# Kernel tuning notes

Measured on AMD Instinct MI355X. Metric: run time of the kernel, lower is better.

## Reference

```python
import jax, jax.numpy as jnp
import numpy as np

SIGMA = 1.0


def _sq_dists(a, b):
    # ||a_i - b_j||^2 via gemm: (n_a, n_b)
    aa = jnp.sum(a * a, axis=1)[:, None]
    bb = jnp.sum(b * b, axis=1)[None, :]
    ab = a @ b.T
    return jnp.maximum(aa + bb - 2.0 * ab, 0.0)


def _rbf(a, b, sigma):
    return jnp.exp(-_sq_dists(a, b) / (2.0 * sigma * sigma))


def setup_inputs() -> dict:
    key = jax.random.key(0)
    kx, ky = jax.random.split(key)
    x = jax.random.normal(kx, (4096, 1024), dtype=jnp.float32)
    y = jax.random.normal(ky, (4096, 1024), dtype=jnp.float32)
    return {"x": x, "y": y}


def reference(x, y):
    # Flatten non-batch dims (module accepts (n, f1, f2, ...))
    xf = x.reshape(x.shape[0], -1)
    yf = y.reshape(y.shape[0], -1)
    n = xf.shape[0]
    m = yf.shape[0]

    k_xx = _rbf(xf, xf, SIGMA)
    k_yy = _rbf(yf, yf, SIGMA)
    k_xy = _rbf(xf, yf, SIGMA)

    # Unbiased estimator: exclude diagonal of k_xx / k_yy
    sum_xx = jnp.sum(k_xx) - jnp.trace(k_xx)
    sum_yy = jnp.sum(k_yy) - jnp.trace(k_yy)
    sum_xy = jnp.sum(k_xy)

    mmd2 = (sum_xx / (n * (n - 1))
            + sum_yy / (m * (m - 1))
            - 2.0 * sum_xy / (n * m))
    return mmd2
```

## Files before the change

### kernel.cpp

```cpp
#include <hip/hip_runtime.h>


#define NROWS 4096
#define KDIM  1024
#define BM 128
#define BN 256
#define NTI 32
#define NTJ 16
#define XY  512
#define TRIB 272

typedef unsigned short u16;
typedef unsigned char  u8;
typedef __attribute__((ext_vector_type(8))) int   int8v;
typedef __attribute__((ext_vector_type(4))) int   int4v;
typedef __attribute__((ext_vector_type(8))) short short8;
typedef __attribute__((ext_vector_type(4))) float f32x4;

__global__ void mmd_zero_sums(float* sums) {
    if (threadIdx.x < 3) sums[threadIdx.x] = 0.0f;
}

__device__ __forceinline__ void async_copy16(const void* g, void* l) {
    __builtin_amdgcn_global_load_lds(
        (const __attribute__((address_space(1))) unsigned int*)g,
        (__attribute__((address_space(3))) unsigned int*)l, 16, 0, 0);
}

__global__ __launch_bounds__(256) void mmd_prep8v(const float* __restrict__ x,
                                                  const float* __restrict__ y,
                                                  float* __restrict__ aa,
                                                  float* __restrict__ bb,
                                                  u8* __restrict__ xb,
                                                  u8* __restrict__ yb,
                                                  float* __restrict__ sums) {
    if (blockIdx.x == 0 && blockIdx.y == 0 && threadIdx.x < 3)
        sums[threadIdx.x] = 0.0f;
    const int w = threadIdx.x >> 6;
    const int l = threadIdx.x & 63;
    const int row = blockIdx.x * 4 + w;
    const float* src = blockIdx.y ? y : x;
    float* ndst = blockIdx.y ? bb : aa;
    u8* bdst    = blockIdx.y ? yb : xb;

    const float4* rp = (const float4*)(src + (size_t)row * KDIM);
    float4 v[4];
    #pragma unroll
    for (int p = 0; p < 4; p++) v[p] = rp[l * 4 + p];

    int pk[4];
    float s = 0.0f;
    #pragma unroll
    for (int p = 0; p < 4; p++) {
        int q = 0;
        q = __builtin_amdgcn_cvt_pk_fp8_f32(v[p].x, v[p].y, q, false);
        q = __builtin_amdgcn_cvt_pk_fp8_f32(v[p].z, v[p].w, q, true);
        pk[p] = q;
        s += v[p].x * v[p].x + v[p].y * v[p].y + v[p].z * v[p].z + v[p].w * v[p].w;
    }
    ((int4v*)(bdst + (size_t)row * KDIM))[l] = (int4v){pk[0], pk[1], pk[2], pk[3]};

    #pragma unroll
    for (int off = 32; off; off >>= 1) s += __shfl_down(s, off, 64);
    if (l == 0) ndst[row] = s;
}

__global__ __launch_bounds__(512, 2) void mmd_tile_fp8(const u8* __restrict__ xb,
                                                       const u8* __restrict__ yb,
                                                       const float* __restrict__ aa,
                                                       const float* __restrict__ bb,
                                                       float* __restrict__ sums) {
    int mode, ti, tj;
    const int bid = blockIdx.x;
    if (bid < XY) {
        mode = 2;
        const int st = bid >> 4;
        const int wi = bid & 15;
        ti = (st >> 2) * 4 + (wi >> 2);
        tj = (st & 3) * 4 + (wi & 3);
    } else {
        int s = bid - XY;
        mode = (s >= TRIB) ? 1 : 0;
        if (s >= TRIB) s -= TRIB;
        int p = (int)(16.5f - sqrtf(272.25f - (float)s));
        if (p < 0) p = 0;
        if (p > 15) p = 15;
        while (p > 0 && p * (33 - p) > s) p--;
        while (p < 15 && (p + 1) * (32 - p) <= s) p++;
        const int r0 = s - p * (33 - p);
        const int wdt = 16 - p;
        ti = 2 * p + (r0 >= wdt ? 1 : 0);
        tj = p + (r0 >= wdt ? r0 - wdt : r0);
    }

    const u8*    __restrict__ A  = (mode == 1) ? yb : xb;
    const u8*    __restrict__ B  = (mode == 0) ? xb : yb;
    const float* __restrict__ na = (mode == 1) ? bb : aa;
    const float* __restrict__ nb = (mode == 0) ? aa : bb;

    __shared__ u8 As[2 * BM * 128];
    __shared__ u8 Bs[2 * BN * 128];
    __shared__ float red[8];

    const int t = threadIdx.x;
    const int w = t >> 6;
    const int l = t & 63;

    const int lrow = l >> 3;
    const int gch  = (l & 7) ^ lrow;
    const u8* aS[2]; const u8* bS[4]; int lA[2], lB[4];
    #pragma unroll
    for (int a = 0; a < 2; a++) {
        const int blk = a * 8 + w;
        aS[a] = A + (size_t)(ti * BM + blk * 8 + lrow) * KDIM + gch * 16;
        lA[a] = blk * 1024 + l * 16;
    }
    #pragma unroll
    for (int b = 0; b < 4; b++) {
        const int blk = b * 8 + w;
        bS[b] = B + (size_t)(tj * BN + blk * 8 + lrow) * KDIM + gch * 16;
        lB[b] = blk * 1024 + l * 16;
    }

    const int wm = (w >> 2) * 64;
    const int wn = (w & 3) * 64;
    const int r  = l & 15;
    const int h  = l >> 4;
    const int s0 = (2 * h) ^ (r & 7);
    const int aB0 = (wm + r) * 128 + s0 * 16;
    const int bB0 = (wn + r) * 128 + s0 * 16;

    f32x4 acc[4][4] = {};

    auto stage = [&](int kt, int dbuf) {
        const int k0 = kt * 128;
        u8* ad = As + dbuf * (BM * 128);
        u8* bd = Bs + dbuf * (BN * 128);
        #pragma unroll
        for (int a = 0; a < 2; a++) async_copy16(aS[a] + k0, ad + lA[a]);
        #pragma unroll
        for (int b = 0; b < 4; b++) async_copy16(bS[b] + k0, bd + lB[b]);
    };

    auto compute = [&](int cbuf) {
        const u8* Ab = As + cbuf * (BM * 128);
        const u8* Bb = Bs + cbuf * (BN * 128);
        int8v bf[4];
        #pragma unroll
        for (int in = 0; in < 4; in++) {
            union { int8v v; int4v hh[2]; } u;
            u.hh[0] = *(const int4v*)(Bb + (bB0 + in * 2048));
            u.hh[1] = *(const int4v*)(Bb + ((bB0 + in * 2048) ^ 16));
            bf[in] = u.v;
        }
        #pragma unroll
        for (int im = 0; im < 4; im++) {
            union { int8v v; int4v hh[2]; } u;
            u.hh[0] = *(const int4v*)(Ab + (aB0 + im * 2048));
            u.hh[1] = *(const int4v*)(Ab + ((aB0 + im * 2048) ^ 16));
            const int8v af = u.v;
            #pragma unroll
            for (int in = 0; in < 4; in++)
                acc[im][in] = __builtin_amdgcn_mfma_scale_f32_16x16x128_f8f6f4(
                    af, bf[in], acc[im][in],
                    0, 0,
                    0, 127,
                    0, 127);
        }
    };

    stage(0, 0);
    __syncthreads();
    int c = 0;
    for (int kt = 1; kt < 8; ++kt) {
        stage(kt, c ^ 1);
        compute(c);
        __syncthreads();
        c ^= 1;
    }
    compute(c);

    const int giBase = ti * BM + wm + h * 4;
    const int gjBase = tj * BN + wn + r;
    float nav[4][4], nbv[4];
    #pragma unroll
    for (int im = 0; im < 4; im++)
        #pragma unroll
        for (int rr = 0; rr < 4; rr++) nav[im][rr] = na[giBase + im * 16 + rr];
    #pragma unroll
    for (int in = 0; in < 4; in++) nbv[in] = nb[gjBase + in * 16];

    float lsum = 0.0f;
    #pragma unroll
    for (int im = 0; im < 4; im++) {
        #pragma unroll
        for (int in = 0; in < 4; in++) {
            const int gj = gjBase + in * 16;
            #pragma unroll
            for (int rr = 0; rr < 4; rr++) {
                const int gi = giBase + im * 16 + rr;
                float d = fmaxf(nav[im][rr] + nbv[in] - 2.0f * acc[im][in][rr], 0.0f);
                float v = __expf(-0.5f * d);
                float wgt = (mode == 2) ? 1.0f : ((gj > gi) ? 2.0f : 0.0f);
                lsum = fmaf(wgt, v, lsum);
            }
        }
    }
    #pragma unroll
    for (int off = 32; off; off >>= 1) lsum += __shfl_down(lsum, off, 64);
    if (l == 0) red[w] = lsum;
    __syncthreads();
    if (t == 0) {
        float bs = red[0] + red[1] + red[2] + red[3]
                 + red[4] + red[5] + red[6] + red[7];
        atomicAdd(&sums[mode], bs);
    }
}

__device__ __forceinline__ unsigned pk_bf16(float lo, float hi) {
    unsigned ul = __float_as_uint(lo); ul += 0x7fffu + ((ul >> 16) & 1u);
    unsigned uh = __float_as_uint(hi); uh += 0x7fffu + ((uh >> 16) & 1u);
    return (ul >> 16) | (uh & 0xffff0000u);
}

__global__ __launch_bounds__(256) void mmd_row_norms(const float* __restrict__ x,
                                                     const float* __restrict__ y,
                                                     float* __restrict__ aa,
                                                     float* __restrict__ bb) {
    const int row = blockIdx.x;
    const float* src = blockIdx.y ? y : x;
    float* dst = blockIdx.y ? bb : aa;
    const float4 v = ((const float4*)(src + (size_t)row * KDIM))[threadIdx.x];
    float s = v.x * v.x + v.y * v.y + v.z * v.z + v.w * v.w;
    #pragma unroll
    for (int off = 32; off; off >>= 1) s += __shfl_down(s, off, 64);
    __shared__ float ws[4];
    if ((threadIdx.x & 63) == 0) ws[threadIdx.x >> 6] = s;
    __syncthreads();
    if (threadIdx.x == 0) dst[row] = ws[0] + ws[1] + ws[2] + ws[3];
}

#define FBM 128
#define LDST 40
#define BK 32
__global__ __launch_bounds__(256) void mmd_tile_v2(const float* __restrict__ x,
                                                   const float* __restrict__ y,
                                                   const float* __restrict__ aa,
                                                   const float* __restrict__ bb,
                                                   float* __restrict__ sums) {
    const int mode = blockIdx.z;
    const int ti = blockIdx.y, tj = blockIdx.x;
    if (mode < 2 && tj < ti) return;
    const float* __restrict__ A  = (mode == 1) ? y : x;
    const float* __restrict__ B  = (mode == 0) ? x : y;
    const float* __restrict__ na = (mode == 1) ? bb : aa;
    const float* __restrict__ nb = (mode == 0) ? aa : bb;
    __shared__ u16 As[FBM * LDST];
    __shared__ u16 Bs[FBM * LDST];
    const int t = threadIdx.x;
    const int srow = t >> 1;
    const int skb  = (t & 1) * 16;
    const float* aptr = A + (size_t)(ti * FBM + srow) * KDIM + skb;
    const float* bptr = B + (size_t)(tj * FBM + srow) * KDIM + skb;
    u16* aDst = &As[srow * LDST + skb];
    u16* bDst = &Bs[srow * LDST + skb];
    const int l  = t & 63;
    const int wv = t >> 6;
    const int wm = (wv >> 1) * 64;
    const int wn = (wv & 1) * 64;
    const int q  = l >> 4;
    const int c  = l & 15;
    const u16* aFrag = &As[(wm + c) * LDST + q * 8];
    const u16* bFrag = &Bs[(wn + c) * LDST + q * 8];
    f32x4 acc[4][4] = {};
    float4 pa[4], pb[4];
    #pragma unroll
    for (int i = 0; i < 4; i++) {
        pa[i] = *(const float4*)(aptr + i * 4);
        pb[i] = *(const float4*)(bptr + i * 4);
    }
    for (int k0 = 0; k0 < KDIM; k0 += BK) {
        uint4 w0, w1;
        w0.x = pk_bf16(pa[0].x, pa[0].y); w0.y = pk_bf16(pa[0].z, pa[0].w);
        w0.z = pk_bf16(pa[1].x, pa[1].y); w0.w = pk_bf16(pa[1].z, pa[1].w);
        w1.x = pk_bf16(pa[2].x, pa[2].y); w1.y = pk_bf16(pa[2].z, pa[2].w);
        w1.z = pk_bf16(pa[3].x, pa[3].y); w1.w = pk_bf16(pa[3].z, pa[3].w);
        __syncthreads();
        ((uint4*)aDst)[0] = w0; ((uint4*)aDst)[1] = w1;
        w0.x = pk_bf16(pb[0].x, pb[0].y); w0.y = pk_bf16(pb[0].z, pb[0].w);
        w0.z = pk_bf16(pb[1].x, pb[1].y); w0.w = pk_bf16(pb[1].z, pb[1].w);
        w1.x = pk_bf16(pb[2].x, pb[2].y); w1.y = pk_bf16(pb[2].z, pb[2].w);
        w1.z = pk_bf16(pb[3].x, pb[3].y); w1.w = pk_bf16(pb[3].z, pb[3].w);
        ((uint4*)bDst)[0] = w0; ((uint4*)bDst)[1] = w1;
        __syncthreads();
        if (k0 + BK < KDIM) {
            #pragma unroll
            for (int i = 0; i < 4; i++) {
                pa[i] = *(const float4*)(aptr + k0 + BK + i * 4);
                pb[i] = *(const float4*)(bptr + k0 + BK + i * 4);
            }
        }
        short8 af[4], bf[4];
        #pragma unroll
        for (int im = 0; im < 4; im++) af[im] = *(const short8*)(aFrag + im * 16 * LDST);
        #pragma unroll
        for (int in = 0; in < 4; in++) bf[in] = *(const short8*)(bFrag + in * 16 * LDST);
        #pragma unroll
        for (int im = 0; im < 4; im++)
            #pragma unroll
            for (int in = 0; in < 4; in++)
                acc[im][in] = __builtin_amdgcn_mfma_f32_16x16x32_bf16(af[im], bf[in], acc[im][in], 0, 0, 0);
    }
    const int giBase = ti * FBM + wm + q * 4;
    const int gjBase = tj * FBM + wn + c;
    float lsum = 0.0f;
    #pragma unroll
    for (int im = 0; im < 4; im++) {
        #pragma unroll
        for (int in = 0; in < 4; in++) {
            const int gj = gjBase + in * 16;
            #pragma unroll
            for (int rr = 0; rr < 4; rr++) {
                const int gi = giBase + im * 16 + rr;
                float d = fmaxf(na[gi] + nb[gj] - 2.0f * acc[im][in][rr], 0.0f);
                float v = __expf(-0.5f * d);
                float wgt = (mode == 2) ? 1.0f : ((gj > gi) ? 2.0f : 0.0f);
                lsum = fmaf(wgt, v, lsum);
            }
        }
    }
    #pragma unroll
    for (int off = 32; off; off >>= 1) lsum += __shfl_down(lsum, off, 64);
    __shared__ float red[4];
    if (l == 0) red[wv] = lsum;
    __syncthreads();
    if (t == 0) atomicAdd(&sums[mode], red[0] + red[1] + red[2] + red[3]);
}

__global__ void mmd_finalize(const float* __restrict__ sums, float* __restrict__ out, int n, int m) {
    if (threadIdx.x == 0) {
        float fn = (float)n, fm = (float)m;
        out[0] = sums[0] / (fn * (fn - 1.0f))
               + sums[1] / (fm * (fm - 1.0f))
               - 2.0f * sums[2] / (fn * fm);
    }
}

extern "C" void kernel_launch(void* const* d_in, const int* in_sizes, int n_in,
                              void* d_out, int out_size, void* d_ws, size_t ws_size,
                              hipStream_t stream) {
    const float* x = (const float*)d_in[0];
    const float* y = (const float*)d_in[1];
    float* out = (float*)d_out;

    char* ws = (char*)d_ws;
    float* aa   = (float*)(ws);
    float* bb   = (float*)(ws + 16384);
    float* sums = (float*)(ws + 32768);
    u8*    xb   = (u8*)(ws + 33024);
    u8*    yb   = xb + (size_t)NROWS * KDIM;

    const size_t needed = 33024 + 2 * (size_t)NROWS * KDIM;
    const int n = in_sizes[0] / KDIM;
    const int m = in_sizes[1] / KDIM;

    if (ws_size >= needed) {
        hipLaunchKernelGGL(mmd_prep8v, dim3(NROWS / 4, 2), dim3(256), 0, stream,
                           x, y, aa, bb, xb, yb, sums);
        hipLaunchKernelGGL(mmd_tile_fp8, dim3(XY + 2 * TRIB), dim3(512), 0, stream,
                           xb, yb, aa, bb, sums);
    } else {
        hipLaunchKernelGGL(mmd_zero_sums, dim3(1), dim3(64), 0, stream, sums);
        hipLaunchKernelGGL(mmd_row_norms, dim3(NROWS, 2), dim3(256), 0, stream, x, y, aa, bb);
        hipLaunchKernelGGL(mmd_tile_v2, dim3(NROWS / FBM, NROWS / FBM, 3), dim3(256), 0, stream,
                           x, y, aa, bb, sums);
    }
    hipLaunchKernelGGL(mmd_finalize, dim3(1), dim3(1), 0, stream, sums, out, n, m);
}
```

Measured before the change: 135.2 us.

## Restructure fp8 MFMA main loop into ping-pong phases and swizzle block order

Replaces the stage/compute loop with an explicit schedule. Each k-step issues the next stage's async LDS copies, waits with a manual vmcnt, then splits its MFMAs into four quadrant phases separated by s_barrier with s_setprio raised around the MFMA groups, so waves interleave memory and matrix work. It also remaps blockIdx across 8 groups of 132 blocks (likely one per XCD) so neighbouring tiles share L2. The risk is that the manual waitcnt and barrier placement is fragile: the removed __syncthreads after compute could leave an LDS write-after-read hazard, and the extra barriers add overhead.

Result: slower. 142.4 us (+5.4%).

```diff
diff --git a/kernel.cpp b/kernel.cpp
--- a/kernel.cpp
+++ b/kernel.cpp
@@ -5,8 +5,6 @@
 #define KDIM  1024
 #define BM 128
 #define BN 256
-#define NTI 32
-#define NTJ 16
 #define XY  512
 #define TRIB 272
 
@@ -70,8 +68,9 @@
                                                        const float* __restrict__ aa,
                                                        const float* __restrict__ bb,
                                                        float* __restrict__ sums) {
+    const int bid = (blockIdx.x & 7) * 132 + (blockIdx.x >> 3);
+
     int mode, ti, tj;
-    const int bid = blockIdx.x;
     if (bid < XY) {
         mode = 2;
         const int st = bid >> 4;
@@ -131,54 +130,80 @@
     const int bB0 = (wn + r) * 128 + s0 * 16;
 
     f32x4 acc[4][4] = {};
-
-    auto stage = [&](int kt, int dbuf) {
-        const int k0 = kt * 128;
-        u8* ad = As + dbuf * (BM * 128);
-        u8* bd = Bs + dbuf * (BN * 128);
-        #pragma unroll
-        for (int a = 0; a < 2; a++) async_copy16(aS[a] + k0, ad + lA[a]);
-        #pragma unroll
-        for (int b = 0; b < 4; b++) async_copy16(bS[b] + k0, bd + lB[b]);
-    };
-
-    auto compute = [&](int cbuf) {
-        const u8* Ab = As + cbuf * (BM * 128);
-        const u8* Bb = Bs + cbuf * (BN * 128);
-        int8v bf[4];
-        #pragma unroll
-        for (int in = 0; in < 4; in++) {
-            union { int8v v; int4v hh[2]; } u;
-            u.hh[0] = *(const int4v*)(Bb + (bB0 + in * 2048));
-            u.hh[1] = *(const int4v*)(Bb + ((bB0 + in * 2048) ^ 16));
-            bf[in] = u.v;
+    int8v af[4], bf[4];
+
+#define STAGE_ALL(KT, DB)                                                   \
+    {                                                                       \
+        u8* ad_ = As + (DB) * (BM * 128);                                   \
+        u8* bd_ = Bs + (DB) * (BN * 128);                                   \
+        const int k0_ = (KT) * 128;                                         \
+        _Pragma("unroll")                                                   \
+        for (int a = 0; a < 2; a++) async_copy16(aS[a] + k0_, ad_ + lA[a]); \
+        _Pragma("unroll")                                                   \
+        for (int b = 0; b < 4; b++) async_copy16(bS[b] + k0_, bd_ + lB[b]); \
+    }
+
+#define LOADA(I)                                                   \
+    { union { int8v v; int4v hh[2]; } u_;                          \
+      u_.hh[0] = *(const int4v*)(Ac + (aB0 + (I) * 2048));         \
+      u_.hh[1] = *(const int4v*)(Ac + ((aB0 + (I) * 2048) ^ 16));  \
+      af[I] = u_.v; }
+
+#define LOADB(I)                                                   \
+    { union { int8v v; int4v hh[2]; } u_;                          \
+      u_.hh[0] = *(const int4v*)(Bc + (bB0 + (I) * 2048));         \
+      u_.hh[1] = *(const int4v*)(Bc + ((bB0 + (I) * 2048) ^ 16));  \
+      bf[I] = u_.v; }
+
+#define MF(IM, IN)                                                          \
+    acc[IM][IN] = __builtin_amdgcn_mfma_scale_f32_16x16x128_f8f6f4(         \
+        af[IM], bf[IN], acc[IM][IN], 0, 0, 0, 127, 0, 127);
+
+    STAGE_ALL(0, 0);
+
+    for (int kt = 0; kt < 8; ++kt) {
+        const int c = kt & 1;
+        const u8* Ac = As + c * (BM * 128);
+        const u8* Bc = Bs + c * (BN * 128);
+
+        if (kt < 7) {
+            STAGE_ALL(kt + 1, c ^ 1);
+            asm volatile("s_waitcnt vmcnt(6)" ::: "memory");
+        } else {
+            asm volatile("s_waitcnt vmcnt(0)" ::: "memory");
         }
-        #pragma unroll
-        for (int im = 0; im < 4; im++) {
-            union { int8v v; int4v hh[2]; } u;
-            u.hh[0] = *(const int4v*)(Ab + (aB0 + im * 2048));
-            u.hh[1] = *(const int4v*)(Ab + ((aB0 + im * 2048) ^ 16));
-            const int8v af = u.v;
-            #pragma unroll
-            for (int in = 0; in < 4; in++)
-                acc[im][in] = __builtin_amdgcn_mfma_scale_f32_16x16x128_f8f6f4(
-                    af, bf[in], acc[im][in],
-                    0, 0,
-                    0, 127,
-                    0, 127);
-        }
-    };
-
-    stage(0, 0);
-    __syncthreads();
-    int c = 0;
-    for (int kt = 1; kt < 8; ++kt) {
-        stage(kt, c ^ 1);
-        compute(c);
-        __syncthreads();
-        c ^= 1;
-    }
-    compute(c);
+        __builtin_amdgcn_sched_barrier(0);
+        __builtin_amdgcn_s_barrier();
+        __builtin_amdgcn_sched_barrier(0);
+
+        LOADA(0) LOADA(1) LOADB(0) LOADB(1)
+        __builtin_amdgcn_s_setprio(1);
+        MF(0, 0) MF(0, 1) MF(1, 0) MF(1, 1)
+        __builtin_amdgcn_s_setprio(0);
+        __builtin_amdgcn_s_barrier();
+
+        LOADB(2) LOADB(3)
+        __builtin_amdgcn_s_setprio(1);
+        MF(0, 2) MF(0, 3) MF(1, 2) MF(1, 3)
+        __builtin_amdgcn_s_setprio(0);
+        __builtin_amdgcn_s_barrier();
+
+        LOADA(2) LOADA(3)
+        __builtin_amdgcn_s_setprio(1);
+        MF(2, 0) MF(2, 1) MF(3, 0) MF(3, 1)
+        __builtin_amdgcn_s_setprio(0);
+        __builtin_amdgcn_s_barrier();
+
+        __builtin_amdgcn_s_setprio(1);
+        MF(2, 2) MF(2, 3) MF(3, 2) MF(3, 3)
+        __builtin_amdgcn_s_setprio(0);
+        __builtin_amdgcn_s_barrier();
+    }
+
+#undef STAGE_ALL
+#undef LOADA
+#undef LOADB
+#undef MF
 
     const int giBase = ti * BM + wm + h * 4;
     const int gjBase = tj * BN + wn + r;
```
